# Kernel tuning notes

Measured on AMD Instinct MI355X. Metric: run time of the kernel, lower is better.

Reference implementation:

```python
import jax, jax.numpy as jnp
import numpy as np

B, D = 16384, 512
EPS_COS = 1e-8  # torch cosine_similarity eps


def setup_inputs() -> dict:
    key = jax.random.key(0)
    ks = jax.random.split(key, 8)
    rep1 = jax.random.normal(ks[0], (B, D), jnp.float32)
    rep2 = jax.random.normal(ks[1], (B, D), jnp.float32)
    rep3 = jax.random.normal(ks[2], (B, D), jnp.float32)
    hazard = jax.random.normal(ks[3], (B, 1), jnp.float32)
    # F.nll_loss expects log-probabilities
    score = jax.nn.log_softmax(jax.random.normal(ks[4], (B, 2), jnp.float32), axis=-1)
    time = jax.random.uniform(ks[5], (B,), jnp.float32)
    event = jax.random.randint(ks[6], (B,), 0, 2, dtype=jnp.int32)
    perm = jax.random.permutation(ks[7], B)  # deterministic stand-in for shuffle()
    x1_idx = perm[: B // 2].astype(jnp.int32)
    x2_idx = perm[B // 2 :].astype(jnp.int32)
    return dict(rep1=rep1, rep2=rep2, rep3=rep3, hazard=hazard, score=score,
                time=time, event=event, x1_idx=x1_idx, x2_idx=x2_idx)


def _normalize(r):
    n = jnp.maximum(jnp.linalg.norm(r, axis=-1, keepdims=True), EPS_COS)
    return r / n


def reference(rep1, rep2, rep3, hazard, score, time, event, x1_idx, x2_idx):
    trade_off, margin, alpha, beta = 0.3, 0.2, 0.5, 0.5
    ev_f = event.astype(score.dtype)

    # ---- cross-entropy term: F.nll_loss(log_probs, event) ----
    nll = -jnp.mean(jnp.take_along_axis(score, event[:, None].astype(jnp.int32), axis=1))

    # ---- Cox negative log-likelihood ----
    order = jnp.argsort(-time)            # descending time
    risk = hazard[order, 0]               # [B]
    evs = ev_f[order]
    log_risk = jnp.log(jnp.cumsum(jnp.exp(risk)) + 1e-6)
    cox = -jnp.sum((risk - log_risk) * evs) / (jnp.sum(evs) + 1e-6)

    # ---- contrastive loss (3 modalities, vectorized over pairs) ----
    R = jnp.stack([_normalize(rep1), _normalize(rep2), _normalize(rep3)])  # [M,B,D]
    x = R[:, x1_idx]  # [M,P,D]
    y = R[:, x2_idx]  # [M,P,D]
    pairs = [(0, 1), (0, 2), (1, 2)]
    dis_xx = sum((x[i] * x[j]).sum(-1) for i, j in pairs)  # [P]
    dis_yy = sum((y[i] * y[j]).sum(-1) for i, j in pairs)  # [P]
    dis_xy = (x * y).sum(-1).sum(0)                         # [P]
    con = jnp.mean(jnp.log1p(jnp.exp(margin + dis_xy - alpha * dis_xx - beta * dis_yy)))

    return nll + cox + trade_off * con
```

## Files before the change

kernel.cpp:

```cpp
#include <hip/hip_runtime.h>
#include <math.h>

#define B_N     16384
#define D_N     512
#define NPAIR   8192
#define NBUCKET 8192
#define COX_BLOCKS 64
#define CON_BLOCKS 2048
#define FUSE_BLOCKS (COX_BLOCKS + CON_BLOCKS)
#define STAT_BLOCKS 64

__device__ __forceinline__ float wave_reduce(float v) {
    #pragma unroll
    for (int m = 32; m >= 1; m >>= 1) v += __shfl_xor(v, m, 64);
    return v;
}

__device__ __forceinline__ float dot4(float4 a, float4 b) {
    return a.x*b.x + a.y*b.y + a.z*b.z + a.w*b.w;
}

__device__ __forceinline__ int bucket_of(float t) {
    return min(max((int)(t * 8192.0f), 0), NBUCKET - 1);
}

__device__ __forceinline__ unsigned long long key_of(float t, int i) {
    return (((unsigned long long)__float_as_uint(t)) << 14) |
           (unsigned long long)(B_N - 1 - i);
}

__global__ __launch_bounds__(256) void k_stats(
        const float* __restrict__ hazard,
        const float* __restrict__ score,
        const float* __restrict__ time,
        const int*   __restrict__ event,
        float* __restrict__ partNll,
        float* __restrict__ partEv,
        float* __restrict__ sumE,
        int*   __restrict__ head,
        int*   __restrict__ next)
{
    __shared__ float sh0[4], sh1[4];
    const int tid  = threadIdx.x;
    const int lane = tid & 63;
    const int wave = tid >> 6;
    const int sb   = blockIdx.x;
    const int i    = sb * 256 + tid;

    const float t = time[i];
    const float e = __expf(hazard[i]);
    const int   b = bucket_of(t);
    atomicAdd(&sumE[b], e);
    const int old = atomicExch(&head[b], i + 1);
    next[i] = old;

    const int ev = event[i];
    float nll_p = wave_reduce(score[i * 2 + ev]);
    float ev_p  = wave_reduce((float)ev);
    if (lane == 0) { sh0[wave] = nll_p; sh1[wave] = ev_p; }
    __syncthreads();
    if (tid == 0) {
        partNll[sb] = sh0[0] + sh0[1] + sh0[2] + sh0[3];
        partEv[sb]  = sh1[0] + sh1[1] + sh1[2] + sh1[3];
    }
}

__global__ __launch_bounds__(256) void k_scan(
        const float* __restrict__ sumE,
        float* __restrict__ cumG)
{
    __shared__ float psum[256];
    const int tid  = threadIdx.x;
    const int base = tid * 32;
    float fs = 0.f;
    #pragma unroll
    for (int k = 0; k < 32; ++k) fs += sumE[base + k];
    psum[tid] = fs;
    __syncthreads();
    for (int d = 1; d < 256; d <<= 1) {
        float v = (tid >= d) ? psum[tid - d] : 0.f;
        __syncthreads();
        psum[tid] += v;
        __syncthreads();
    }
    const float total = psum[255];
    float run = total - psum[tid];
    #pragma unroll
    for (int k = 31; k >= 0; --k) {
        cumG[base + k] = run;
        run += sumE[base + k];
    }
}

__global__ __launch_bounds__(256) void k_fused(
        const float* __restrict__ rep1,
        const float* __restrict__ rep2,
        const float* __restrict__ rep3,
        const float* __restrict__ hazard,
        const float* __restrict__ time,
        const int*   __restrict__ event,
        const int*   __restrict__ x1_idx,
        const int*   __restrict__ x2_idx,
        const int*   __restrict__ head,
        const int*   __restrict__ next,
        const float* __restrict__ cumG,
        float* __restrict__ partCon,
        float* __restrict__ partCox)
{
    __shared__ float shX[4];
    const int tid  = threadIdx.x;
    const int lane = tid & 63;
    const int wave = tid >> 6;

    if (blockIdx.x >= COX_BLOCKS) {
        const int p  = (blockIdx.x - COX_BLOCKS) * 4 + wave;
        const int ia = x1_idx[p];
        const int ib = x2_idx[p];
        const float4* A1 = (const float4*)(rep1 + (size_t)ia * D_N);
        const float4* A2 = (const float4*)(rep2 + (size_t)ia * D_N);
        const float4* A3 = (const float4*)(rep3 + (size_t)ia * D_N);
        const float4* B1 = (const float4*)(rep1 + (size_t)ib * D_N);
        const float4* B2 = (const float4*)(rep2 + (size_t)ib * D_N);
        const float4* B3 = (const float4*)(rep3 + (size_t)ib * D_N);

        const int k0 = lane;
        const int k1 = lane + 64;
        float4 a1_0 = A1[k0], a2_0 = A2[k0], a3_0 = A3[k0];
        float4 b1_0 = B1[k0], b2_0 = B2[k0], b3_0 = B3[k0];
        float4 a1_1 = A1[k1], a2_1 = A2[k1], a3_1 = A3[k1];
        float4 b1_1 = B1[k1], b2_1 = B2[k1], b3_1 = B3[k1];

        float v[15];
        #pragma unroll
        for (int k = 0; k < 15; ++k) v[k] = 0.f;
        v[0]  += dot4(a1_0, a1_0); v[1]  += dot4(a2_0, a2_0); v[2]  += dot4(a3_0, a3_0);
        v[3]  += dot4(b1_0, b1_0); v[4]  += dot4(b2_0, b2_0); v[5]  += dot4(b3_0, b3_0);
        v[6]  += dot4(a1_0, a2_0); v[7]  += dot4(a1_0, a3_0); v[8]  += dot4(a2_0, a3_0);
        v[9]  += dot4(b1_0, b2_0); v[10] += dot4(b1_0, b3_0); v[11] += dot4(b2_0, b3_0);
        v[12] += dot4(a1_0, b1_0); v[13] += dot4(a2_0, b2_0); v[14] += dot4(a3_0, b3_0);
        v[0]  += dot4(a1_1, a1_1); v[1]  += dot4(a2_1, a2_1); v[2]  += dot4(a3_1, a3_1);
        v[3]  += dot4(b1_1, b1_1); v[4]  += dot4(b2_1, b2_1); v[5]  += dot4(b3_1, b3_1);
        v[6]  += dot4(a1_1, a2_1); v[7]  += dot4(a1_1, a3_1); v[8]  += dot4(a2_1, a3_1);
        v[9]  += dot4(b1_1, b2_1); v[10] += dot4(b1_1, b3_1); v[11] += dot4(b2_1, b3_1);
        v[12] += dot4(a1_1, b1_1); v[13] += dot4(a2_1, b2_1); v[14] += dot4(a3_1, b3_1);

        #pragma unroll
        for (int k = 0; k < 15; ++k) v[k] = wave_reduce(v[k]);

        if (lane == 0) {
            float n1a = fmaxf(sqrtf(v[0]), 1e-8f), n2a = fmaxf(sqrtf(v[1]), 1e-8f), n3a = fmaxf(sqrtf(v[2]), 1e-8f);
            float n1b = fmaxf(sqrtf(v[3]), 1e-8f), n2b = fmaxf(sqrtf(v[4]), 1e-8f), n3b = fmaxf(sqrtf(v[5]), 1e-8f);
            float dxx = v[6]/(n1a*n2a) + v[7]/(n1a*n3a) + v[8]/(n2a*n3a);
            float dyy = v[9]/(n1b*n2b) + v[10]/(n1b*n3b) + v[11]/(n2b*n3b);
            float dxy = v[12]/(n1a*n1b) + v[13]/(n2a*n2b) + v[14]/(n3a*n3b);
            float s = 0.2f + dxy - 0.5f*dxx - 0.5f*dyy;
            shX[wave] = log1pf(expf(s));
        }
        __syncthreads();
        if (tid == 0)
            partCon[blockIdx.x - COX_BLOCKS] = shX[0] + shX[1] + shX[2] + shX[3];
    } else {
        const int i = blockIdx.x * 256 + tid;
        const float t = time[i];
        const float h = hazard[i];
        const int   b = bucket_of(t);
        const unsigned long long ki = key_of(t, i);

        float cum = cumG[b] + __expf(h);
        int p = head[b];
        while (p >= 1 && p <= B_N) {
            const int j = p - 1;
            const float tj = time[j];
            if (key_of(tj, j) > ki) cum += __expf(hazard[j]);
            p = next[j];
        }
        float cox_p = event[i] ? (h - logf(cum + 1e-6f)) : 0.f;
        cox_p = wave_reduce(cox_p);
        if (lane == 0) shX[wave] = cox_p;
        __syncthreads();
        if (tid == 0)
            partCox[blockIdx.x] = shX[0] + shX[1] + shX[2] + shX[3];
    }
}

__global__ __launch_bounds__(256) void k_final(
        const float* __restrict__ partCon,
        const float* __restrict__ partCox,
        const float* __restrict__ partNll,
        const float* __restrict__ partEv,
        float* __restrict__ out)
{
    __shared__ float shX[4];
    const int tid  = threadIdx.x;
    const int lane = tid & 63;
    const int wave = tid >> 6;

    float con = 0.f;
    #pragma unroll
    for (int k = 0; k < CON_BLOCKS / 256; ++k) con += partCon[tid + k * 256];
    float cox = 0.f, nll = 0.f, ev = 0.f;
    if (tid < COX_BLOCKS) {
        cox = partCox[tid];
        nll = partNll[tid];
        ev  = partEv[tid];
    }
    con = wave_reduce(con);
    cox = wave_reduce(cox);
    nll = wave_reduce(nll);
    ev  = wave_reduce(ev);
    __syncthreads();
    if (lane == 0) { shX[wave] = con; }
    __syncthreads();
    float C = shX[0] + shX[1] + shX[2] + shX[3];
    if (lane == 0) { shX[wave] = cox; }
    __syncthreads();
    float X = shX[0] + shX[1] + shX[2] + shX[3];
    if (lane == 0) { shX[wave] = nll; }
    __syncthreads();
    float N = shX[0] + shX[1] + shX[2] + shX[3];
    if (lane == 0) { shX[wave] = ev; }
    __syncthreads();
    float E = shX[0] + shX[1] + shX[2] + shX[3];
    if (tid == 0)
        out[0] = (-N / (float)B_N) + (-X / (E + 1e-6f)) + 0.3f * (C / (float)NPAIR);
}

extern "C" void kernel_launch(void* const* d_in, const int* in_sizes, int n_in,
                              void* d_out, int out_size, void* d_ws, size_t ws_size,
                              hipStream_t stream)
{
    const float* rep1   = (const float*)d_in[0];
    const float* rep2   = (const float*)d_in[1];
    const float* rep3   = (const float*)d_in[2];
    const float* hazard = (const float*)d_in[3];
    const float* score  = (const float*)d_in[4];
    const float* time_  = (const float*)d_in[5];
    const int*   event  = (const int*)d_in[6];
    const int*   x1     = (const int*)d_in[7];
    const int*   x2     = (const int*)d_in[8];
    float* out = (float*)d_out;

    char* w = (char*)d_ws;
    float*    sumE    = (float*)   (w + 0);
    int*      head    = (int*)     (w + 32768);
    int*      next    = (int*)     (w + 65600);
    float*    partCon = (float*)   (w + 131136);
    float*    partNll = (float*)   (w + 139328);
    float*    partEv  = (float*)   (w + 139584);
    float*    partCox = (float*)   (w + 139840);
    float*    cumG    = (float*)   (w + 140096);

    k_stats <<<STAT_BLOCKS, 256, 0, stream>>>(hazard, score, time_, event,
                                              partNll, partEv, sumE, head, next);
    k_scan  <<<1, 256, 0, stream>>>(sumE, cumG);
    k_fused <<<FUSE_BLOCKS, 256, 0, stream>>>(rep1, rep2, rep3, hazard, time_, event,
                                              x1, x2, head, next, cumG,
                                              partCon, partCox);
    k_final <<<1, 256, 0, stream>>>(partCon, partCox, partNll, partEv, out);
}
```

Measured before the change: 141.2 us.

## Precompute per-row norms and intra-row dots in a separate prestat pass

Adds blocks to the stats kernel that compute per-row squared norms and cross-modality dots for all rows, stored in a rowStat buffer. The pair kernel then only computes the three x·y dots and reads the row stats instead of doing 15 reductions. This reduces reductions in the pair kernel, but the embeddings are now streamed twice, once in prestat and again in the pair kernel, which adds memory traffic.

```diff
diff --git a/kernel.cpp b/kernel.cpp
--- a/kernel.cpp
+++ b/kernel.cpp
@@ -9,6 +9,8 @@
 #define CON_BLOCKS 2048
 #define FUSE_BLOCKS (COX_BLOCKS + CON_BLOCKS)
 #define STAT_BLOCKS 64
+#define PRE_BLOCKS  4096
+#define PRESTAT_BLOCKS (STAT_BLOCKS + PRE_BLOCKS)
 
 __device__ __forceinline__ float wave_reduce(float v) {
     #pragma unroll
@@ -29,7 +31,10 @@
            (unsigned long long)(B_N - 1 - i);
 }
 
-__global__ __launch_bounds__(256) void k_stats(
+__global__ __launch_bounds__(256) void k_prestat(
+        const float* __restrict__ rep1,
+        const float* __restrict__ rep2,
+        const float* __restrict__ rep3,
         const float* __restrict__ hazard,
         const float* __restrict__ score,
         const float* __restrict__ time,
@@ -38,30 +43,55 @@
         float* __restrict__ partEv,
         float* __restrict__ sumE,
         int*   __restrict__ head,
-        int*   __restrict__ next)
+        int*   __restrict__ next,
+        float* __restrict__ rowStat)
 {
     __shared__ float sh0[4], sh1[4];
     const int tid  = threadIdx.x;
     const int lane = tid & 63;
     const int wave = tid >> 6;
-    const int sb   = blockIdx.x;
-    const int i    = sb * 256 + tid;
-
-    const float t = time[i];
-    const float e = __expf(hazard[i]);
-    const int   b = bucket_of(t);
-    atomicAdd(&sumE[b], e);
-    const int old = atomicExch(&head[b], i + 1);
-    next[i] = old;
-
-    const int ev = event[i];
-    float nll_p = wave_reduce(score[i * 2 + ev]);
-    float ev_p  = wave_reduce((float)ev);
-    if (lane == 0) { sh0[wave] = nll_p; sh1[wave] = ev_p; }
-    __syncthreads();
-    if (tid == 0) {
-        partNll[sb] = sh0[0] + sh0[1] + sh0[2] + sh0[3];
-        partEv[sb]  = sh1[0] + sh1[1] + sh1[2] + sh1[3];
+
+    if (blockIdx.x < STAT_BLOCKS) {
+        const int sb = blockIdx.x;
+        const int i  = sb * 256 + tid;
+        const float t = time[i];
+        const float e = __expf(hazard[i]);
+        const int   b = bucket_of(t);
+        atomicAdd(&sumE[b], e);
+        const int old = atomicExch(&head[b], i + 1);
+        next[i] = old;
+
+        const int ev = event[i];
+        float nll_p = wave_reduce(score[i * 2 + ev]);
+        float ev_p  = wave_reduce((float)ev);
+        if (lane == 0) { sh0[wave] = nll_p; sh1[wave] = ev_p; }
+        __syncthreads();
+        if (tid == 0) {
+            partNll[sb] = sh0[0] + sh0[1] + sh0[2] + sh0[3];
+            partEv[sb]  = sh1[0] + sh1[1] + sh1[2] + sh1[3];
+        }
+    } else {
+        const int r = (blockIdx.x - STAT_BLOCKS) * 4 + wave;
+        const float4* R1 = (const float4*)(rep1 + (size_t)r * D_N);
+        const float4* R2 = (const float4*)(rep2 + (size_t)r * D_N);
+        const float4* R3 = (const float4*)(rep3 + (size_t)r * D_N);
+        const int k0 = lane;
+        const int k1 = lane + 64;
+        float4 r1_0 = R1[k0], r2_0 = R2[k0], r3_0 = R3[k0];
+        float4 r1_1 = R1[k1], r2_1 = R2[k1], r3_1 = R3[k1];
+
+        float s11 = 0.f, s22 = 0.f, s33 = 0.f, d12 = 0.f, d13 = 0.f, d23 = 0.f;
+        s11 += dot4(r1_0, r1_0); s22 += dot4(r2_0, r2_0); s33 += dot4(r3_0, r3_0);
+        d12 += dot4(r1_0, r2_0); d13 += dot4(r1_0, r3_0); d23 += dot4(r2_0, r3_0);
+        s11 += dot4(r1_1, r1_1); s22 += dot4(r2_1, r2_1); s33 += dot4(r3_1, r3_1);
+        d12 += dot4(r1_1, r2_1); d13 += dot4(r1_1, r3_1); d23 += dot4(r2_1, r3_1);
+        s11 = wave_reduce(s11); s22 = wave_reduce(s22); s33 = wave_reduce(s33);
+        d12 = wave_reduce(d12); d13 = wave_reduce(d13); d23 = wave_reduce(d23);
+        if (lane == 0) {
+            float* st = rowStat + (size_t)r * 6;
+            st[0] = s11; st[1] = s22; st[2] = s33;
+            st[3] = d12; st[4] = d13; st[5] = d23;
+        }
     }
 }
 
@@ -104,6 +134,7 @@
         const int*   __restrict__ head,
         const int*   __restrict__ next,
         const float* __restrict__ cumG,
+        const float* __restrict__ rowStat,
         float* __restrict__ partCon,
         float* __restrict__ partCox)
 {
@@ -130,29 +161,19 @@
         float4 a1_1 = A1[k1], a2_1 = A2[k1], a3_1 = A3[k1];
         float4 b1_1 = B1[k1], b2_1 = B2[k1], b3_1 = B3[k1];
 
-        float v[15];
-        #pragma unroll
-        for (int k = 0; k < 15; ++k) v[k] = 0.f;
-        v[0]  += dot4(a1_0, a1_0); v[1]  += dot4(a2_0, a2_0); v[2]  += dot4(a3_0, a3_0);
-        v[3]  += dot4(b1_0, b1_0); v[4]  += dot4(b2_0, b2_0); v[5]  += dot4(b3_0, b3_0);
-        v[6]  += dot4(a1_0, a2_0); v[7]  += dot4(a1_0, a3_0); v[8]  += dot4(a2_0, a3_0);
-        v[9]  += dot4(b1_0, b2_0); v[10] += dot4(b1_0, b3_0); v[11] += dot4(b2_0, b3_0);
-        v[12] += dot4(a1_0, b1_0); v[13] += dot4(a2_0, b2_0); v[14] += dot4(a3_0, b3_0);
-        v[0]  += dot4(a1_1, a1_1); v[1]  += dot4(a2_1, a2_1); v[2]  += dot4(a3_1, a3_1);
-        v[3]  += dot4(b1_1, b1_1); v[4]  += dot4(b2_1, b2_1); v[5]  += dot4(b3_1, b3_1);
-        v[6]  += dot4(a1_1, a2_1); v[7]  += dot4(a1_1, a3_1); v[8]  += dot4(a2_1, a3_1);
-        v[9]  += dot4(b1_1, b2_1); v[10] += dot4(b1_1, b3_1); v[11] += dot4(b2_1, b3_1);
-        v[12] += dot4(a1_1, b1_1); v[13] += dot4(a2_1, b2_1); v[14] += dot4(a3_1, b3_1);
-
-        #pragma unroll
-        for (int k = 0; k < 15; ++k) v[k] = wave_reduce(v[k]);
+        float v12 = 0.f, v13 = 0.f, v14 = 0.f;
+        v12 += dot4(a1_0, b1_0); v13 += dot4(a2_0, b2_0); v14 += dot4(a3_0, b3_0);
+        v12 += dot4(a1_1, b1_1); v13 += dot4(a2_1, b2_1); v14 += dot4(a3_1, b3_1);
+        v12 = wave_reduce(v12); v13 = wave_reduce(v13); v14 = wave_reduce(v14);
 
         if (lane == 0) {
-            float n1a = fmaxf(sqrtf(v[0]), 1e-8f), n2a = fmaxf(sqrtf(v[1]), 1e-8f), n3a = fmaxf(sqrtf(v[2]), 1e-8f);
-            float n1b = fmaxf(sqrtf(v[3]), 1e-8f), n2b = fmaxf(sqrtf(v[4]), 1e-8f), n3b = fmaxf(sqrtf(v[5]), 1e-8f);
-            float dxx = v[6]/(n1a*n2a) + v[7]/(n1a*n3a) + v[8]/(n2a*n3a);
-            float dyy = v[9]/(n1b*n2b) + v[10]/(n1b*n3b) + v[11]/(n2b*n3b);
-            float dxy = v[12]/(n1a*n1b) + v[13]/(n2a*n2b) + v[14]/(n3a*n3b);
+            const float* sa = rowStat + (size_t)ia * 6;
+            const float* sbb = rowStat + (size_t)ib * 6;
+            float n1a = fmaxf(sqrtf(sa[0]), 1e-8f),  n2a = fmaxf(sqrtf(sa[1]), 1e-8f),  n3a = fmaxf(sqrtf(sa[2]), 1e-8f);
+            float n1b = fmaxf(sqrtf(sbb[0]), 1e-8f), n2b = fmaxf(sqrtf(sbb[1]), 1e-8f), n3b = fmaxf(sqrtf(sbb[2]), 1e-8f);
+            float dxx = sa[3]/(n1a*n2a)  + sa[4]/(n1a*n3a)  + sa[5]/(n2a*n3a);
+            float dyy = sbb[3]/(n1b*n2b) + sbb[4]/(n1b*n3b) + sbb[5]/(n2b*n3b);
+            float dxy = v12/(n1a*n1b) + v13/(n2a*n2b) + v14/(n3a*n3b);
             float s = 0.2f + dxy - 0.5f*dxx - 0.5f*dyy;
             shX[wave] = log1pf(expf(s));
         }
@@ -249,12 +270,14 @@
     float*    partEv  = (float*)   (w + 139584);
     float*    partCox = (float*)   (w + 139840);
     float*    cumG    = (float*)   (w + 140096);
-
-    k_stats <<<STAT_BLOCKS, 256, 0, stream>>>(hazard, score, time_, event,
-                                              partNll, partEv, sumE, head, next);
-    k_scan  <<<1, 256, 0, stream>>>(sumE, cumG);
-    k_fused <<<FUSE_BLOCKS, 256, 0, stream>>>(rep1, rep2, rep3, hazard, time_, event,
-                                              x1, x2, head, next, cumG,
-                                              partCon, partCox);
-    k_final <<<1, 256, 0, stream>>>(partCon, partCox, partNll, partEv, out);
-}
+    float*    rowStat = (float*)   (w + 172864);
+
+    k_prestat <<<PRESTAT_BLOCKS, 256, 0, stream>>>(rep1, rep2, rep3, hazard, score,
+                                                   time_, event, partNll, partEv,
+                                                   sumE, head, next, rowStat);
+    k_scan    <<<1, 256, 0, stream>>>(sumE, cumG);
+    k_fused   <<<FUSE_BLOCKS, 256, 0, stream>>>(rep1, rep2, rep3, hazard, time_, event,
+                                                x1, x2, head, next, cumG, rowStat,
+                                                partCon, partCox);
+    k_final   <<<1, 256, 0, stream>>>(partCon, partCox, partNll, partEv, out);
+}
```

New measurement: 154.0 us. 9.1% more time.
